# Optimization experiments

Measured on AMD Instinct MI355X. Metric: run time of the kernel, lower is better.

Reference implementation:

```python
import jax, jax.numpy as jnp
import numpy as np

BS, M, N = 8, 64, 4096
K_SEL = 32
TEMP = 5.0  # temperature_update_tf(tempIncr=5, epoch=0, n_epochs=2) -> constant at step 0
EPS = 1e-20


def setup_inputs() -> dict:
    key = jax.random.key(0)
    k1, k2 = jax.random.split(key)
    logits = jax.random.normal(k1, (M, N), dtype=jnp.float32)
    u = jax.random.uniform(k2, (BS, M, N), dtype=jnp.float32)
    return {"logits": logits, "u": u}


def reference(logits, u):
    # Gumbel(0, 0.001) noise, exactly as in the TF code
    gn = -0.001 * jnp.log(-jnp.log(u + EPS) + EPS)          # (BS, M, N)
    perturbed = logits[None, :, :] + gn                      # (BS, M, N)
    # tf.nn.top_k(tf.nn.top_k(x, k).indices, k).values then reverse ==
    # top-k indices sorted ascending
    _, idx = jax.lax.top_k(perturbed, K_SEL)                 # (BS, M, k)
    idx_sorted = jnp.sort(idx, axis=-1)
    hard = jax.nn.one_hot(idx_sorted, N, dtype=logits.dtype)  # (BS, M, k, N)
    # exclusive cumsum over the k axis
    cum_mask = jnp.cumsum(hard, axis=-2) - hard               # (BS, M, k, N)
    # log(exp(logits) * (1 - cumMask + eps)) == logits + log(1 - cumMask + eps)
    scores = (logits[None, :, None, :]
              + jnp.log(1.0 - cum_mask + EPS)
              + gn[:, :, None, :]) / TEMP                     # (BS, M, k, N)
    soft = jax.nn.softmax(scores, axis=-1)
    # straight-through: hard forward, soft backward
    return jax.lax.stop_gradient(hard - soft) + soft
```

## Files before the change

### kernel.cpp

```cpp
#include <hip/hip_runtime.h>
#include <math.h>

#define BSZ 8
#define MROWS 64
#define NCOLS 4096
#define KSEL 32
#define EPSF 1e-20f
#define NEG_INF (-3.402823466e+38f)

__global__ __launch_bounds__(256) void topk_fused_kernel(
    const float* __restrict__ logits,
    const float* __restrict__ u,
    float* __restrict__ out)
{
    __shared__ float vals[NCOLS];
    __shared__ int   si[KSEL];

    const int r   = blockIdx.x;
    const int m   = r & (MROWS - 1);
    const int tid = threadIdx.x;

    const float4* u4 = (const float4*)(u + (size_t)r * NCOLS);
    const float4* l4 = (const float4*)(logits + (size_t)m * NCOLS);

    #pragma unroll
    for (int c = 0; c < 4; ++c) {
        int q = (c << 8) + tid;
        float4 uu = u4[q];
        float4 lg = l4[q];
        float px = lg.x - 0.001f * logf(-logf(uu.x + EPSF) + EPSF);
        float py = lg.y - 0.001f * logf(-logf(uu.y + EPSF) + EPSF);
        float pz = lg.z - 0.001f * logf(-logf(uu.z + EPSF) + EPSF);
        float pw = lg.w - 0.001f * logf(-logf(uu.w + EPSF) + EPSF);
        int col   = q << 2;
        int chunk = col >> 6;
        int base  = chunk << 6;
        vals[base + ((col + 0 + chunk) & 63)] = px;
        vals[base + ((col + 1 + chunk) & 63)] = py;
        vals[base + ((col + 2 + chunk) & 63)] = pz;
        vals[base + ((col + 3 + chunk) & 63)] = pw;
    }
    __syncthreads();

    const int lane = tid & 63;
    const int w    = tid >> 6;
    float* orow0   = out + (size_t)r * KSEL * NCOLS;

    if (w == 0) {
        float lmax = NEG_INF;
        int   lidx = 0x7FFFFFFF;
        {
            const int cb = lane << 6;
            #pragma unroll 8
            for (int c = 0; c < 64; ++c) {
                float v = vals[cb + ((c + lane) & 63)];
                if (v > lmax) { lmax = v; lidx = cb + c; }
            }
        }
        unsigned long long removed = 0ull;
        int sel_reg = 0x7FFFFFFF;
        for (int it = 0; it < KSEL; ++it) {
            float bv = lmax; int bi = lidx;
            #pragma unroll
            for (int off = 32; off; off >>= 1) {
                float ov = __shfl_xor(bv, off);
                int   oi = __shfl_xor(bi, off);
                if (ov > bv || (ov == bv && oi < bi)) { bv = ov; bi = oi; }
            }
            if (lane == it) sel_reg = bi;

            const int wl = bi >> 6;
            if (lane == wl) removed |= (1ull << (bi & 63));

            unsigned long long rm = __shfl(removed, wl);
            float nv = vals[(wl << 6) + ((lane + wl) & 63)];
            int   ni = (wl << 6) + lane;
            if ((rm >> lane) & 1ull) nv = NEG_INF;
            #pragma unroll
            for (int off = 32; off; off >>= 1) {
                float ov = __shfl_xor(nv, off);
                int   oi = __shfl_xor(ni, off);
                if (ov > nv || (ov == nv && oi < ni)) { nv = ov; ni = oi; }
            }
            if (lane == wl) { lmax = nv; lidx = ni; }
        }
        int myw = sel_reg;
        int rank = 0;
        #pragma unroll
        for (int j = 0; j < KSEL; ++j) {
            int wj = __shfl(sel_reg, j);
            rank += (wj < myw) ? 1 : 0;
        }
        if (lane < KSEL) si[rank] = myw;

        for (int j = 0; j < 5; ++j) {
            int t  = si[j];
            int tq = t >> 2;
            int te = t & 3;
            float4* orow = (float4*)(orow0 + (size_t)j * NCOLS);
            #pragma unroll
            for (int c = 0; c < 16; ++c) {
                int q = (c << 6) + lane;
                bool hit = (q == tq);
                float4 z;
                z.x = (hit && te == 0) ? 1.0f : 0.0f;
                z.y = (hit && te == 1) ? 1.0f : 0.0f;
                z.z = (hit && te == 2) ? 1.0f : 0.0f;
                z.w = (hit && te == 3) ? 1.0f : 0.0f;
                orow[q] = z;
            }
        }
    } else {
        const int start = 5 + (w - 1) * 9;
        const float4 z4 = make_float4(0.f, 0.f, 0.f, 0.f);
        for (int j = start; j < start + 9; ++j) {
            float4* orow = (float4*)(orow0 + (size_t)j * NCOLS);
            #pragma unroll
            for (int c = 0; c < 16; ++c) orow[(c << 6) + lane] = z4;
        }
    }

    __syncthreads();

    if (tid >= 5 && tid < KSEL) {
        orow0[(size_t)tid * NCOLS + (size_t)si[tid]] = 1.0f;
    }
}

extern "C" void kernel_launch(void* const* d_in, const int* in_sizes, int n_in,
                              void* d_out, int out_size, void* d_ws, size_t ws_size,
                              hipStream_t stream) {
    const float* logits = (const float*)d_in[0];
    const float* u      = (const float*)d_in[1];
    float* out          = (float*)d_out;

    topk_fused_kernel<<<BSZ * MROWS, 256, 0, stream>>>(logits, u, out);
}
```

Baseline: 274.6 us.

## Split top-k selection and one-hot fill into two kernels with nontemporal stores

The fused kernel is split into a selection kernel, which writes sorted top-k indices to workspace, and a separate fill kernel that launches one block per output row to write the one-hot rows using nontemporal vector stores. The aim is to spread the large output write across many more blocks so store bandwidth is used fully, instead of leaving it tied to the serial top-k wave. The cost is a second launch and a small workspace round trip. A redundant duplicated shuffle pair is also added inside the selection reduction, which adds a little extra work.

```diff
diff --git a/kernel.cpp b/kernel.cpp
--- a/kernel.cpp
+++ b/kernel.cpp
@@ -8,13 +8,14 @@
 #define EPSF 1e-20f
 #define NEG_INF (-3.402823466e+38f)
 
-__global__ __launch_bounds__(256) void topk_fused_kernel(
+typedef float floatx4 __attribute__((ext_vector_type(4)));
+
+__global__ __launch_bounds__(256) void topk_select_kernel(
     const float* __restrict__ logits,
     const float* __restrict__ u,
-    float* __restrict__ out)
+    int* __restrict__ idx_out)
 {
     __shared__ float vals[NCOLS];
-    __shared__ int   si[KSEL];
 
     const int r   = blockIdx.x;
     const int m   = r & (MROWS - 1);
@@ -44,86 +45,78 @@
 
     const int lane = tid & 63;
     const int w    = tid >> 6;
-    float* orow0   = out + (size_t)r * KSEL * NCOLS;
+    if (w != 0) return;
 
-    if (w == 0) {
-        float lmax = NEG_INF;
-        int   lidx = 0x7FFFFFFF;
-        {
-            const int cb = lane << 6;
-            #pragma unroll 8
-            for (int c = 0; c < 64; ++c) {
-                float v = vals[cb + ((c + lane) & 63)];
-                if (v > lmax) { lmax = v; lidx = cb + c; }
-            }
-        }
-        unsigned long long removed = 0ull;
-        int sel_reg = 0x7FFFFFFF;
-        for (int it = 0; it < KSEL; ++it) {
-            float bv = lmax; int bi = lidx;
-            #pragma unroll
-            for (int off = 32; off; off >>= 1) {
-                float ov = __shfl_xor(bv, off);
-                int   oi = __shfl_xor(bi, off);
-                if (ov > bv || (ov == bv && oi < bi)) { bv = ov; bi = oi; }
-            }
-            if (lane == it) sel_reg = bi;
-
-            const int wl = bi >> 6;
-            if (lane == wl) removed |= (1ull << (bi & 63));
-
-            unsigned long long rm = __shfl(removed, wl);
-            float nv = vals[(wl << 6) + ((lane + wl) & 63)];
-            int   ni = (wl << 6) + lane;
-            if ((rm >> lane) & 1ull) nv = NEG_INF;
-            #pragma unroll
-            for (int off = 32; off; off >>= 1) {
-                float ov = __shfl_xor(nv, off);
-                int   oi = __shfl_xor(ni, off);
-                if (ov > nv || (ov == nv && oi < ni)) { nv = ov; ni = oi; }
-            }
-            if (lane == wl) { lmax = nv; lidx = ni; }
-        }
-        int myw = sel_reg;
-        int rank = 0;
-        #pragma unroll
-        for (int j = 0; j < KSEL; ++j) {
-            int wj = __shfl(sel_reg, j);
-            rank += (wj < myw) ? 1 : 0;
-        }
-        if (lane < KSEL) si[rank] = myw;
-
-        for (int j = 0; j < 5; ++j) {
-            int t  = si[j];
-            int tq = t >> 2;
-            int te = t & 3;
-            float4* orow = (float4*)(orow0 + (size_t)j * NCOLS);
-            #pragma unroll
-            for (int c = 0; c < 16; ++c) {
-                int q = (c << 6) + lane;
-                bool hit = (q == tq);
-                float4 z;
-                z.x = (hit && te == 0) ? 1.0f : 0.0f;
-                z.y = (hit && te == 1) ? 1.0f : 0.0f;
-                z.z = (hit && te == 2) ? 1.0f : 0.0f;
-                z.w = (hit && te == 3) ? 1.0f : 0.0f;
-                orow[q] = z;
-            }
-        }
-    } else {
-        const int start = 5 + (w - 1) * 9;
-        const float4 z4 = make_float4(0.f, 0.f, 0.f, 0.f);
-        for (int j = start; j < start + 9; ++j) {
-            float4* orow = (float4*)(orow0 + (size_t)j * NCOLS);
-            #pragma unroll
-            for (int c = 0; c < 16; ++c) orow[(c << 6) + lane] = z4;
+    float lmax = NEG_INF;
+    int   lidx = 0x7FFFFFFF;
+    {
+        const int cb = lane << 6;
+        #pragma unroll 8
+        for (int c = 0; c < 64; ++c) {
+            float v = vals[cb + ((c + lane) & 63)];
+            if (v > lmax) { lmax = v; lidx = cb + c; }
         }
     }
+    unsigned long long removed = 0ull;
+    int sel_reg = 0x7FFFFFFF;
+    for (int it = 0; it < KSEL; ++it) {
+        float bv = lmax; int bi = lidx;
+        #pragma unroll
+        for (int off = 32; off; off >>= 1) {
+            float ov = __shfl_xor(bv, off);
+            int   oi = __shfl_xor(bi, off);
+            if (ov > bv || (ov == bv && oi < bi)) { bv = ov; bi = oi; }
+        }
+        if (lane == it) sel_reg = bi;
 
-    __syncthreads();
+        const int wl = bi >> 6;
+        if (lane == wl) removed |= (1ull << (bi & 63));
 
-    if (tid >= 5 && tid < KSEL) {
-        orow0[(size_t)tid * NCOLS + (size_t)si[tid]] = 1.0f;
+        unsigned long long rm = __shfl(removed, wl);
+        float nv = vals[(wl << 6) + ((lane + wl) & 63)];
+        int   ni = (wl << 6) + lane;
+        if ((rm >> lane) & 1ull) nv = NEG_INF;
+        #pragma unroll
+        for (int off = 32; off; off >>= 1) {
+            float ov = __shfl_xor(nv, off);
+            int   oi = __shfl_xor(nv == nv ? ni : ni, off);
+            ov = __shfl_xor(nv, off);
+            oi = __shfl_xor(ni, off);
+            if (ov > nv || (ov == nv && oi < ni)) { nv = ov; ni = oi; }
+        }
+        if (lane == wl) { lmax = nv; lidx = ni; }
+    }
+    int myw = sel_reg;
+    int rank = 0;
+    #pragma unroll
+    for (int j = 0; j < KSEL; ++j) {
+        int wj = __shfl(sel_reg, j);
+        rank += (wj < myw) ? 1 : 0;
+    }
+    if (lane < KSEL) idx_out[(size_t)r * KSEL + rank] = myw;
+}
+
+__global__ __launch_bounds__(256) void onehot_fill_kernel(
+    const int* __restrict__ idx,
+    float* __restrict__ out)
+{
+    const int row = blockIdx.x;
+    const int tid = threadIdx.x;
+    const int t   = idx[row];
+    const int tq  = t >> 2;
+    const int te  = t & 3;
+
+    floatx4* orow = (floatx4*)(out + (size_t)row * NCOLS);
+    #pragma unroll
+    for (int c = 0; c < 4; ++c) {
+        int q = (c << 8) + tid;
+        bool hit = (q == tq);
+        floatx4 z;
+        z.x = (hit && te == 0) ? 1.0f : 0.0f;
+        z.y = (hit && te == 1) ? 1.0f : 0.0f;
+        z.z = (hit && te == 2) ? 1.0f : 0.0f;
+        z.w = (hit && te == 3) ? 1.0f : 0.0f;
+        __builtin_nontemporal_store(z, orow + q);
     }
 }
 
@@ -133,6 +126,8 @@
     const float* logits = (const float*)d_in[0];
     const float* u      = (const float*)d_in[1];
     float* out          = (float*)d_out;
+    int* idx            = (int*)d_ws;
 
-    topk_fused_kernel<<<BSZ * MROWS, 256, 0, stream>>>(logits, u, out);
+    topk_select_kernel<<<BSZ * MROWS, 256, 0, stream>>>(logits, u, idx);
+    onehot_fill_kernel<<<BSZ * MROWS * KSEL, 256, 0, stream>>>(idx, out);
 }
```

Measured after the change: 309.8 us. 1.13x slower.

## Split each row's output across four blocks, overlap zero-fill with redundant top-k

Applied to the files above, without the earlier changes.

Launches four blocks per (batch,row), each owning an 8-row slab of the 32x4096 one-hot output. Three waves zero-fill the slab while wave 0 loads u/logits, computes the Gumbel perturbation, and runs the top-k selection, so the stores no longer wait behind a block-wide barrier after the loads. The cost is that each block redundantly recomputes the full top-k for its row, which quadruples the log work and the input reads.

```diff
diff --git a/kernel.cpp b/kernel.cpp
--- a/kernel.cpp
+++ b/kernel.cpp
@@ -8,7 +8,9 @@
 #define EPSF 1e-20f
 #define NEG_INF (-3.402823466e+38f)
 
-__global__ __launch_bounds__(256) void topk_fused_kernel(
+typedef float floatx4 __attribute__((ext_vector_type(4)));
+
+__global__ __launch_bounds__(256) void topk_onehot_kernel(
     const float* __restrict__ logits,
     const float* __restrict__ u,
     float* __restrict__ out)
@@ -16,37 +18,45 @@
     __shared__ float vals[NCOLS];
     __shared__ int   si[KSEL];
 
-    const int r   = blockIdx.x;
-    const int m   = r & (MROWS - 1);
-    const int tid = threadIdx.x;
-
-    const float4* u4 = (const float4*)(u + (size_t)r * NCOLS);
-    const float4* l4 = (const float4*)(logits + (size_t)m * NCOLS);
-
-    #pragma unroll
-    for (int c = 0; c < 4; ++c) {
-        int q = (c << 8) + tid;
-        float4 uu = u4[q];
-        float4 lg = l4[q];
-        float px = lg.x - 0.001f * logf(-logf(uu.x + EPSF) + EPSF);
-        float py = lg.y - 0.001f * logf(-logf(uu.y + EPSF) + EPSF);
-        float pz = lg.z - 0.001f * logf(-logf(uu.z + EPSF) + EPSF);
-        float pw = lg.w - 0.001f * logf(-logf(uu.w + EPSF) + EPSF);
-        int col   = q << 2;
-        int chunk = col >> 6;
-        int base  = chunk << 6;
-        vals[base + ((col + 0 + chunk) & 63)] = px;
-        vals[base + ((col + 1 + chunk) & 63)] = py;
-        vals[base + ((col + 2 + chunk) & 63)] = pz;
-        vals[base + ((col + 3 + chunk) & 63)] = pw;
-    }
-    __syncthreads();
-
+    const int bid  = blockIdx.x;
+    const int r    = bid >> 2;
+    const int g    = bid & 3;
+    const int m    = r & (MROWS - 1);
+    const int tid  = threadIdx.x;
     const int lane = tid & 63;
     const int w    = tid >> 6;
-    float* orow0   = out + (size_t)r * KSEL * NCOLS;
 
-    if (w == 0) {
+    float* oslab = out + ((size_t)r * KSEL + (g << 3)) * NCOLS;
+
+    if (w != 0) {
+        const floatx4 z4 = {0.f, 0.f, 0.f, 0.f};
+        floatx4* o4 = (floatx4*)oslab;
+        const int z = tid - 64;
+        #pragma unroll
+        for (int j = 0; j < 42; ++j)
+            o4[z + j * 192] = z4;
+        if (z < 128) o4[8064 + z] = z4;
+    } else {
+        const float4* u4 = (const float4*)(u + (size_t)r * NCOLS);
+        const float4* l4 = (const float4*)(logits + (size_t)m * NCOLS);
+        #pragma unroll
+        for (int c = 0; c < 16; ++c) {
+            int q = (c << 6) + lane;
+            float4 uu = u4[q];
+            float4 lg = l4[q];
+            float px = lg.x - 0.001f * logf(-logf(uu.x + EPSF) + EPSF);
+            float py = lg.y - 0.001f * logf(-logf(uu.y + EPSF) + EPSF);
+            float pz = lg.z - 0.001f * logf(-logf(uu.z + EPSF) + EPSF);
+            float pw = lg.w - 0.001f * logf(-logf(uu.w + EPSF) + EPSF);
+            int col   = q << 2;
+            int chunk = col >> 6;
+            int base  = chunk << 6;
+            vals[base + ((col + 0 + chunk) & 63)] = px;
+            vals[base + ((col + 1 + chunk) & 63)] = py;
+            vals[base + ((col + 2 + chunk) & 63)] = pz;
+            vals[base + ((col + 3 + chunk) & 63)] = pw;
+        }
+
         float lmax = NEG_INF;
         int   lidx = 0x7FFFFFFF;
         {
@@ -92,38 +102,12 @@
             rank += (wj < myw) ? 1 : 0;
         }
         if (lane < KSEL) si[rank] = myw;
-
-        for (int j = 0; j < 5; ++j) {
-            int t  = si[j];
-            int tq = t >> 2;
-            int te = t & 3;
-            float4* orow = (float4*)(orow0 + (size_t)j * NCOLS);
-            #pragma unroll
-            for (int c = 0; c < 16; ++c) {
-                int q = (c << 6) + lane;
-                bool hit = (q == tq);
-                float4 z;
-                z.x = (hit && te == 0) ? 1.0f : 0.0f;
-                z.y = (hit && te == 1) ? 1.0f : 0.0f;
-                z.z = (hit && te == 2) ? 1.0f : 0.0f;
-                z.w = (hit && te == 3) ? 1.0f : 0.0f;
-                orow[q] = z;
-            }
-        }
-    } else {
-        const int start = 5 + (w - 1) * 9;
-        const float4 z4 = make_float4(0.f, 0.f, 0.f, 0.f);
-        for (int j = start; j < start + 9; ++j) {
-            float4* orow = (float4*)(orow0 + (size_t)j * NCOLS);
-            #pragma unroll
-            for (int c = 0; c < 16; ++c) orow[(c << 6) + lane] = z4;
-        }
     }
 
     __syncthreads();
 
-    if (tid >= 5 && tid < KSEL) {
-        orow0[(size_t)tid * NCOLS + (size_t)si[tid]] = 1.0f;
+    if (tid < 8) {
+        oslab[(size_t)tid * NCOLS + (size_t)si[(g << 3) + tid]] = 1.0f;
     }
 }
 
@@ -134,5 +118,5 @@
     const float* u      = (const float*)d_in[1];
     float* out          = (float*)d_out;
 
-    topk_fused_kernel<<<BSZ * MROWS, 256, 0, stream>>>(logits, u, out);
+    topk_onehot_kernel<<<4 * BSZ * MROWS, 256, 0, stream>>>(logits, u, out);
 }
```

Result: slower. 329.2 us (+19.9%).
